# Performance work log

Hardware: AMD Instinct MI355X
Metric: run time of the kernel (lower is better)

Reference implementation:

```python
import jax, jax.numpy as jnp
import numpy as np

N, E, L, H, C, F_IN = 50000, 800000, 3, 8, 16, 128  # nodes, edges, layers, heads, per-head dim, input dim
NEG_SLOPE = 0.2


def setup_inputs() -> dict:
    key = jax.random.key(0)
    k = jax.random.split(key, 8)
    scale = 0.1
    x = jax.random.normal(k[0], (N, F_IN), dtype=jnp.float32)
    Ws = jax.random.normal(k[1], (L, F_IN, H * C), dtype=jnp.float32) * scale
    att_src = jax.random.normal(k[2], (L, H, C), dtype=jnp.float32) * scale
    att_dst = jax.random.normal(k[3], (L, H, C), dtype=jnp.float32) * scale
    biases = jnp.zeros((L, H * C), dtype=jnp.float32)
    fc_w = jax.random.normal(k[4], (H * C, C), dtype=jnp.float32) * scale
    fc_b = jnp.zeros((C,), dtype=jnp.float32)
    edge_index = jax.random.randint(k[5], (2, E), 0, N, dtype=jnp.int64)
    return {"x": x, "Ws": Ws, "att_src": att_src, "att_dst": att_dst,
            "biases": biases, "fc_w": fc_w, "fc_b": fc_b, "edge_index": edge_index}


def _gat_layer(x, W, a_src, a_dst, b, src, dst):
    # x: [N, F]; W: [F, H*C]; a_src/a_dst: [H, C]; src/dst: [E+N] (self-loops included)
    n = x.shape[0]
    h = (x @ W).reshape(n, H, C)                      # [N, H, C]
    e_src = jnp.einsum('nhc,hc->nh', h, a_src)        # [N, H]
    e_dst = jnp.einsum('nhc,hc->nh', h, a_dst)
    e = jax.nn.leaky_relu(e_src[src] + e_dst[dst], NEG_SLOPE)   # [E+N, H]
    # segment softmax over incoming edges of each target node
    emax = jax.ops.segment_max(e, dst, num_segments=n)          # [N, H]
    ex = jnp.exp(e - emax[dst])
    denom = jax.ops.segment_sum(ex, dst, num_segments=n)        # [N, H]
    alpha = ex / (denom[dst] + 1e-16)                            # [E+N, H]
    out = jax.ops.segment_sum(alpha[:, :, None] * h[src], dst, num_segments=n)  # [N, H, C]
    return out.reshape(n, H * C) + b


def reference(x, Ws, att_src, att_dst, biases, fc_w, fc_b, edge_index):
    loop = jnp.arange(N, dtype=edge_index.dtype)
    src = jnp.concatenate([edge_index[0], loop])  # add self-loops (PyG default)
    dst = jnp.concatenate([edge_index[1], loop])
    h = x
    for l in range(L):
        h = _gat_layer(h, Ws[l], att_src[l], att_dst[l], biases[l], src, dst)
        h = jax.nn.elu(h)
    return h @ fc_w + fc_b  # [N, C]
```

## Files before the change

kernel.cpp:

```cpp
#include <hip/hip_runtime.h>
#include <hip/hip_bf16.h>


#define GAT_F 128
#define GAT_H 8
#define GAT_C 16

typedef __attribute__((ext_vector_type(8))) short bf16x8;
typedef __attribute__((ext_vector_type(4))) float f32x4;

__device__ __forceinline__ float bf2f(unsigned short u) {
    union { unsigned int i; float f; } x; x.i = ((unsigned int)u) << 16; return x.f;
}
__device__ __forceinline__ float bfhi2f(unsigned int u) {
    union { unsigned int i; float f; } x; x.i = u & 0xFFFF0000u; return x.f;
}
__device__ __forceinline__ float bflo2f(unsigned int u) {
    union { unsigned int i; float f; } x; x.i = u << 16; return x.f;
}
__device__ __forceinline__ unsigned int pk_bf16(float a, float b) {
    union { float f; unsigned int i; } ua, ub;
    ua.f = a; ub.f = b;
    unsigned int ra = (ua.i + 0x7FFFu + ((ua.i >> 16) & 1u)) >> 16;
    unsigned int rb = (ub.i + 0x7FFFu + ((ub.i >> 16) & 1u)) & 0xFFFF0000u;
    return ra | rb;
}
__device__ __forceinline__ unsigned short f2bf(float a) {
    union { float f; unsigned int i; } ua; ua.f = a;
    return (unsigned short)((ua.i + 0x7FFFu + ((ua.i >> 16) & 1u)) >> 16);
}
__device__ __forceinline__ float ldf(const void* p, size_t i, int isf32) {
    return isf32 ? ((const float*)p)[i] : bf2f(((const unsigned short*)p)[i]);
}
__device__ __forceinline__ int ldei(const int* ei, int i, int is64) {
    return is64 ? ei[2 * (size_t)i] : ei[i];
}

__global__ void k_detect(const unsigned short* __restrict__ xb,
                         const int* __restrict__ ei, int* flags) {
    __shared__ int nan_cnt, zero_cnt;
    if (threadIdx.x == 0) { nan_cnt = 0; zero_cnt = 0; }
    __syncthreads();
    int t = threadIdx.x;
    int ln = 0;
    for (int i = t; i < 8192; i += 256) {
        unsigned short u = xb[i];
        if ((u & 0x7F80) == 0x7F80) ln++;
    }
    int lz = 0;
    for (int i = t; i < 2048; i += 256) {
        if (ei[2 * i + 1] == 0) lz++;
    }
    if (ln) atomicAdd(&nan_cnt, ln);
    if (lz) atomicAdd(&zero_cnt, lz);
    __syncthreads();
    if (t == 0) {
        flags[0] = (nan_cnt > 3) ? 1 : 0;
        flags[1] = (zero_cnt > 1024) ? 1 : 0;
    }
}

__global__ void k_prep(const void* __restrict__ W, const void* __restrict__ asrc,
                       const void* __restrict__ adst,
                       unsigned short* __restrict__ wt, unsigned short* __restrict__ wa,
                       int Lw, const int* __restrict__ flags) {
    int isf32 = flags[0];
    int b = blockIdx.x, t = threadIdx.x;
    if (b < Lw * 64) {
        int gid = b * 256 + t;
        int l = gid >> 14, r = gid & 16383;
        int c = r >> 7, k = r & 127;
        float v = ldf(W, (size_t)l * 16384 + k * 128 + c, isf32);
        wt[gid] = f2bf(v);
    } else {
        int id = (b - Lw * 64) * 256 + t;
        int l = id >> 11, q = id & 2047;
        int j = q >> 7, k = q & 127;
        int head = j & 7;
        const void* av = (j < 8) ? asrc : adst;
        float acc = 0.f;
        #pragma unroll
        for (int cc = 0; cc < 16; cc++) {
            float w = ldf(W, (size_t)l * 16384 + k * 128 + head * 16 + cc, isf32);
            float a = ldf(av, (size_t)l * 128 + head * 16 + cc, isf32);
            acc += w * a;
        }
        wa[id] = f2bf(acc);
    }
}

__global__ void k_init_deg(int* deg, int n) {
    int i = blockIdx.x * 256 + threadIdx.x;
    if (i < n) deg[i] = 1;
}

__global__ void k_count_deg(const int* __restrict__ ei, int* deg, int E,
                            const int* __restrict__ flags) {
    int k = blockIdx.x * 256 + threadIdx.x;
    int is64 = flags[1];
    if (k < E) atomicAdd(&deg[ldei(ei, E + k, is64)], 1);
}

__global__ __launch_bounds__(256) void k_scan_blk(
    const int* __restrict__ deg, int* __restrict__ rp_local,
    int* __restrict__ bsum, int n)
{
    int b = blockIdx.x, t = threadIdx.x;
    int i0 = b * 1024 + t * 4;
    int v0 = 0, v1 = 0, v2 = 0, v3 = 0;
    if (i0 + 3 < n) {
        int4 d = *(const int4*)(deg + i0);
        v0 = d.x; v1 = d.y; v2 = d.z; v3 = d.w;
    } else {
        if (i0     < n) v0 = deg[i0];
        if (i0 + 1 < n) v1 = deg[i0 + 1];
        if (i0 + 2 < n) v2 = deg[i0 + 2];
        if (i0 + 3 < n) v3 = deg[i0 + 3];
    }
    int s = v0 + v1 + v2 + v3;
    int lane = t & 63, wid = t >> 6;
    int sc = s;
    #pragma unroll
    for (int off = 1; off < 64; off <<= 1) {
        int o = __shfl_up(sc, off);
        if (lane >= off) sc += o;
    }
    __shared__ int wsum[4];
    if (lane == 63) wsum[wid] = sc;
    __syncthreads();
    int woff = 0;
    #pragma unroll
    for (int w2 = 0; w2 < 4; w2++) if (w2 < wid) woff += wsum[w2];
    int excl = woff + sc - s;
    if (i0     < n) rp_local[i0]     = excl;
    if (i0 + 1 < n) rp_local[i0 + 1] = excl + v0;
    if (i0 + 2 < n) rp_local[i0 + 2] = excl + v0 + v1;
    if (i0 + 3 < n) rp_local[i0 + 3] = excl + v0 + v1 + v2;
    if (t == 255) bsum[b] = woff + sc;
}

__global__ __launch_bounds__(256) void k_scan_top(
    int* __restrict__ bsum, int* __restrict__ rowptr, int nb, int n)
{
    __shared__ int sh[1024];
    int t = threadIdx.x;
    for (int i = t; i < 1024; i += 256) sh[i] = (i < nb) ? bsum[i] : 0;
    __syncthreads();
    for (int off = 1; off < 1024; off <<= 1) {
        int vals[4];
        #pragma unroll
        for (int k = 0; k < 4; k++) {
            int i = t + 256 * k;
            vals[k] = (i >= off) ? sh[i - off] : 0;
        }
        __syncthreads();
        #pragma unroll
        for (int k = 0; k < 4; k++) sh[t + 256 * k] += vals[k];
        __syncthreads();
    }
    for (int i = t; i < nb; i += 256) bsum[i] = (i == 0) ? 0 : sh[i - 1];
    if (t == 0) rowptr[n] = sh[nb - 1];
}

__global__ void k_place_add(int* __restrict__ rowptr, const int* __restrict__ bsum,
                            int* __restrict__ adj, int* __restrict__ cursor, int n)
{
    int i = blockIdx.x * 256 + threadIdx.x;
    if (i < n) {
        int r = rowptr[i] + bsum[i >> 10];
        rowptr[i] = r;
        adj[r] = i;
        cursor[i] = 1;
    }
    if (blockIdx.x == 0 && threadIdx.x < 8) adj[rowptr[n] + threadIdx.x] = 0;
}

__global__ void k_scatter(const int* __restrict__ ei, const int* __restrict__ rowptr,
                          int* __restrict__ cursor, int* __restrict__ adj, int E,
                          const int* __restrict__ flags) {
    int k = blockIdx.x * 256 + threadIdx.x;
    int is64 = flags[1];
    if (k < E) {
        int s = ldei(ei, k, is64);
        int d = ldei(ei, E + k, is64);
        int p = atomicAdd(&cursor[d], 1);
        adj[rowptr[d] + p] = s;
    }
}

__global__ __launch_bounds__(256) void k_gemm_mfma(
    const void* __restrict__ xin, int x_is_input,
    const unsigned short* __restrict__ wt,
    const unsigned short* __restrict__ wa,
    unsigned int* __restrict__ hb, float* __restrict__ es, float* __restrict__ ed,
    int n, const int* __restrict__ flags)
{
    __shared__ unsigned short xl[64 * 136];
    __shared__ unsigned short wl[144 * 136];
    int isf32 = flags[0];
    int t = threadIdx.x;
    int row0 = blockIdx.x * 64;

    if (isf32 || !x_is_input) {
        const float4* xg = (const float4*)xin;
        for (int i = t; i < 2048; i += 256) {
            int r = i >> 5, c4 = i & 31;
            int gr = row0 + r;
            uint2 u = make_uint2(0u, 0u);
            if (gr < n) {
                float4 v = xg[(size_t)gr * 32 + c4];
                u = make_uint2(pk_bf16(v.x, v.y), pk_bf16(v.z, v.w));
            }
            *(uint2*)&xl[r * 136 + c4 * 4] = u;
        }
    } else {
        const ushort4* xg = (const ushort4*)xin;
        for (int i = t; i < 2048; i += 256) {
            int r = i >> 5, c4 = i & 31;
            int gr = row0 + r;
            ushort4 v = make_ushort4(0, 0, 0, 0);
            if (gr < n) v = xg[(size_t)gr * 32 + c4];
            *(ushort4*)&xl[r * 136 + c4 * 4] = v;
        }
    }
    {
        const ushort4* wg = (const ushort4*)wt;
        for (int i = t; i < 4096; i += 256) {
            int c = i >> 5, k4 = i & 31;
            *(ushort4*)&wl[c * 136 + k4 * 4] = wg[i];
        }
        const ushort4* wag = (const ushort4*)wa;
        for (int i = t; i < 512; i += 256) {
            int j = i >> 5, k4 = i & 31;
            *(ushort4*)&wl[(128 + j) * 136 + k4 * 4] = wag[i];
        }
    }
    __syncthreads();

    int lane = t & 63, wid = t >> 6, quad = lane >> 4, col = lane & 15;
    f32x4 acc[9];
    #pragma unroll
    for (int ct = 0; ct < 9; ct++) acc[ct] = (f32x4){0.f, 0.f, 0.f, 0.f};

    #pragma unroll
    for (int ks = 0; ks < 4; ks++) {
        int k0 = ks * 32;
        bf16x8 af = *(const bf16x8*)&xl[(wid * 16 + col) * 136 + k0 + quad * 8];
        #pragma unroll
        for (int ct = 0; ct < 9; ct++) {
            bf16x8 bf = *(const bf16x8*)&wl[(ct * 16 + col) * 136 + k0 + quad * 8];
            acc[ct] = __builtin_amdgcn_mfma_f32_16x16x32_bf16(af, bf, acc[ct], 0, 0, 0);
        }
    }

    #pragma unroll
    for (int ct = 0; ct < 8; ct++) {
        #pragma unroll
        for (int r = 0; r < 4; r++) {
            int grow = row0 + wid * 16 + quad * 4 + r;
            float v = acc[ct][r];
            float vp = __shfl_xor(v, 1);
            if (!(lane & 1) && grow < n)
                hb[(size_t)grow * 64 + ct * 8 + (col >> 1)] = pk_bf16(v, vp);
        }
    }
    #pragma unroll
    for (int r = 0; r < 4; r++) {
        int grow = row0 + wid * 16 + quad * 4 + r;
        float v = acc[8][r];
        if (grow < n) {
            if (col < 8) es[(size_t)grow * 8 + col] = v;
            else         ed[(size_t)grow * 8 + col - 8] = v;
        }
    }
}

__global__ __launch_bounds__(256) void k_aggregate(
    const unsigned int* __restrict__ hb,
    const float* __restrict__ es, const float* __restrict__ ed,
    const int* __restrict__ rowptr, const int* __restrict__ adj,
    const void* __restrict__ bias, long b_off, float* __restrict__ out, int n,
    const int* __restrict__ flags)
{
    int isf32 = flags[0];
    int lane = threadIdx.x & 63;
    int node = blockIdx.x * 4 + (threadIdx.x >> 6);
    if (node >= n) return;
    int base = rowptr[node];
    int deg = rowptr[node + 1] - base;
    int head = lane >> 3;
    float edv = ed[node * 8 + head];

    float acc0 = 0.f, acc1 = 0.f, lsum = 0.f;
    for (int j0 = 0; j0 < deg; j0 += 4) {
        int sa = adj[base + j0];
        int sb = adj[base + j0 + 1];
        int sc = adj[base + j0 + 2];
        int sd = adj[base + j0 + 3];
        float va = es[sa * 8 + head] + edv;
        float vb = es[sb * 8 + head] + edv;
        float vc = es[sc * 8 + head] + edv;
        float vd = es[sd * 8 + head] + edv;
        unsigned int ha = hb[sa * 64 + lane];
        unsigned int hbv = hb[sb * 64 + lane];
        unsigned int hc = hb[sc * 64 + lane];
        unsigned int hd = hb[sd * 64 + lane];
        va = va > 0.f ? va : 0.2f * va;
        vb = vb > 0.f ? vb : 0.2f * vb;
        vc = vc > 0.f ? vc : 0.2f * vc;
        vd = vd > 0.f ? vd : 0.2f * vd;
        float pa = __expf(va);
        float pb = (j0 + 1 < deg) ? __expf(vb) : 0.f;
        float pc = (j0 + 2 < deg) ? __expf(vc) : 0.f;
        float pd = (j0 + 3 < deg) ? __expf(vd) : 0.f;
        lsum += (pa + pb) + (pc + pd);
        acc0 += pa * bflo2f(ha) + pb * bflo2f(hbv) + pc * bflo2f(hc) + pd * bflo2f(hd);
        acc1 += pa * bfhi2f(ha) + pb * bfhi2f(hbv) + pc * bfhi2f(hc) + pd * bfhi2f(hd);
    }

    float inv = 1.f / (lsum + 1e-16f);
    int ch = lane << 1;
    float o0 = acc0 * inv + ldf(bias, b_off + ch, isf32);
    float o1 = acc1 * inv + ldf(bias, b_off + ch + 1, isf32);
    o0 = o0 > 0.f ? o0 : (__expf(o0) - 1.f);
    o1 = o1 > 0.f ? o1 : (__expf(o1) - 1.f);
    *(float2*)(out + (size_t)node * GAT_F + ch) = make_float2(o0, o1);
}

__global__ __launch_bounds__(256) void k_fc(
    const float* __restrict__ h, const void* __restrict__ fw,
    const void* __restrict__ fb, void* __restrict__ out, int n,
    const int* __restrict__ flags)
{
    __shared__ float fws[GAT_F * GAT_C];
    int isf32 = flags[0];
    int t = threadIdx.x;
    for (int i = t; i < GAT_F * GAT_C; i += 256)
        fws[i] = ldf(fw, i, isf32);
    __syncthreads();
    int row = blockIdx.x * 256 + t;
    if (row >= n) return;
    float acc[16];
    #pragma unroll
    for (int c = 0; c < 16; c++) acc[c] = ldf(fb, c, isf32);
    const float4* hr = (const float4*)(h + (size_t)row * GAT_F);
    for (int k4 = 0; k4 < GAT_F / 4; k4++) {
        float4 xv = hr[k4];
        float xs4[4] = {xv.x, xv.y, xv.z, xv.w};
        #pragma unroll
        for (int kk = 0; kk < 4; kk++) {
            int k = k4 * 4 + kk;
            const float4* wr = (const float4*)(fws + k * GAT_C);
            #pragma unroll
            for (int c4 = 0; c4 < 4; c4++) {
                float4 wv = wr[c4];
                acc[c4 * 4 + 0] += xs4[kk] * wv.x;
                acc[c4 * 4 + 1] += xs4[kk] * wv.y;
                acc[c4 * 4 + 2] += xs4[kk] * wv.z;
                acc[c4 * 4 + 3] += xs4[kk] * wv.w;
            }
        }
    }
    if (isf32) {
        float* o = (float*)out + (size_t)row * GAT_C;
        #pragma unroll
        for (int c = 0; c < 16; c++) o[c] = acc[c];
    } else {
        __hip_bfloat16* o = (__hip_bfloat16*)out + (size_t)row * GAT_C;
        #pragma unroll
        for (int c = 0; c < 16; c++) o[c] = __float2bfloat16(acc[c]);
    }
}

extern "C" void kernel_launch(void* const* d_in, const int* in_sizes, int n_in,
                              void* d_out, int out_size, void* d_ws, size_t ws_size,
                              hipStream_t stream) {
    const void* x      = d_in[0];
    const void* Ws     = d_in[1];
    const void* att_s  = d_in[2];
    const void* att_d  = d_in[3];
    const void* biases = d_in[4];
    const void* fc_w   = d_in[5];
    const void* fc_b   = d_in[6];
    const int*  ei     = (const int*)d_in[7];

    const int N  = in_sizes[0] / GAT_F;
    const int E  = in_sizes[7] / 2;
    const int L  = in_sizes[1] / (GAT_F * GAT_F);
    const int ET = E + N;

    char* w = (char*)d_ws;
    int* flags         = (int*)w;            w += 64;
    float* hA          = (float*)w;          w += (size_t)N * GAT_F * 4;
    unsigned int* hB   = (unsigned int*)w;   w += (size_t)N * 64 * 4;
    float* es          = (float*)w;          w += (size_t)N * GAT_H * 4;
    float* ed          = (float*)w;          w += (size_t)N * GAT_H * 4;
    int* rowptr        = (int*)w;            w += (((size_t)(N + 1) * 4 + 15) & ~15ull);
    int* cursor        = (int*)w;            w += (size_t)N * 4;
    int* bsum          = (int*)w;            w += 1024 * 4;
    int* adj           = (int*)w;            w += (size_t)(ET + 16) * 4;
    unsigned short* wt = (unsigned short*)w; w += (size_t)L * 16384 * 2;
    unsigned short* wa = (unsigned short*)w; w += (size_t)L * 2048 * 2;

    int nb_n = (N + 255) / 256;
    int nb_e = (E + 255) / 256;
    int nb_s = (N + 1023) / 1024;

    k_detect<<<1, 256, 0, stream>>>((const unsigned short*)x, ei, flags);
    k_prep<<<L * 64 + L * 8, 256, 0, stream>>>(Ws, att_s, att_d, wt, wa, L, flags);

    k_init_deg<<<nb_n, 256, 0, stream>>>(cursor, N);
    k_count_deg<<<nb_e, 256, 0, stream>>>(ei, cursor, E, flags);
    k_scan_blk<<<nb_s, 256, 0, stream>>>(cursor, rowptr, bsum, N);
    k_scan_top<<<1, 256, 0, stream>>>(bsum, rowptr, nb_s, N);
    k_place_add<<<nb_n, 256, 0, stream>>>(rowptr, bsum, adj, cursor, N);
    k_scatter<<<nb_e, 256, 0, stream>>>(ei, rowptr, cursor, adj, E, flags);

    int nb_g = (N + 63) / 64;
    int nb_a = (N + 3) / 4;
    for (int l = 0; l < L; l++) {
        k_gemm_mfma<<<nb_g, 256, 0, stream>>>(
            (l == 0) ? x : (const void*)hA, (l == 0) ? 1 : 0,
            wt + (size_t)l * 16384, wa + (size_t)l * 2048,
            hB, es, ed, N, flags);
        k_aggregate<<<nb_a, 256, 0, stream>>>(
            hB, es, ed, rowptr, adj,
            biases, (long)l * GAT_F, hA, N, flags);
    }
    k_fc<<<nb_n, 256, 0, stream>>>(hA, fc_w, fc_b, d_out, N, flags);
}
```

Baseline: 409.0 us.

## Compute per-edge attention weights once per lane and share through LDS

The aggregation kernel now uses one lane per edge to load that edge's source index, gather all 8 head logits with float4 loads, and compute leaky-ReLU and exp for every head. The results go into per-wave LDS buffers. A second inner loop then reads the indices and weights from LDS and gathers the bf16 features as before. This removes the redundant exp and logit gathers that 8 lanes per head used to repeat, and makes the adjacency loads coalesced. The cost is extra LDS traffic, more registers, and a two-phase loop per 64-edge chunk, which relies on intra-wavefront ordering instead of a barrier.

```diff
diff --git a/kernel.cpp b/kernel.cpp
--- a/kernel.cpp
+++ b/kernel.cpp
@@ -282,40 +282,62 @@
     const void* __restrict__ bias, long b_off, float* __restrict__ out, int n,
     const int* __restrict__ flags)
 {
+    __shared__ __align__(16) float alds[4][64 * 12];
+    __shared__ __align__(16) int   slds[4][64];
     int isf32 = flags[0];
     int lane = threadIdx.x & 63;
-    int node = blockIdx.x * 4 + (threadIdx.x >> 6);
+    int wid = threadIdx.x >> 6;
+    int node = blockIdx.x * 4 + wid;
     if (node >= n) return;
     int base = rowptr[node];
     int deg = rowptr[node + 1] - base;
     int head = lane >> 3;
-    float edv = ed[node * 8 + head];
+
+    const float4* es4 = (const float4*)es;
+    const float4* ed4 = (const float4*)ed;
+    float edv[8];
+    {
+        float4 a = ed4[node * 2];
+        float4 b = ed4[node * 2 + 1];
+        edv[0] = a.x; edv[1] = a.y; edv[2] = a.z; edv[3] = a.w;
+        edv[4] = b.x; edv[5] = b.y; edv[6] = b.z; edv[7] = b.w;
+    }
 
     float acc0 = 0.f, acc1 = 0.f, lsum = 0.f;
-    for (int j0 = 0; j0 < deg; j0 += 4) {
-        int sa = adj[base + j0];
-        int sb = adj[base + j0 + 1];
-        int sc = adj[base + j0 + 2];
-        int sd = adj[base + j0 + 3];
-        float va = es[sa * 8 + head] + edv;
-        float vb = es[sb * 8 + head] + edv;
-        float vc = es[sc * 8 + head] + edv;
-        float vd = es[sd * 8 + head] + edv;
-        unsigned int ha = hb[sa * 64 + lane];
-        unsigned int hbv = hb[sb * 64 + lane];
-        unsigned int hc = hb[sc * 64 + lane];
-        unsigned int hd = hb[sd * 64 + lane];
-        va = va > 0.f ? va : 0.2f * va;
-        vb = vb > 0.f ? vb : 0.2f * vb;
-        vc = vc > 0.f ? vc : 0.2f * vc;
-        vd = vd > 0.f ? vd : 0.2f * vd;
-        float pa = __expf(va);
-        float pb = (j0 + 1 < deg) ? __expf(vb) : 0.f;
-        float pc = (j0 + 2 < deg) ? __expf(vc) : 0.f;
-        float pd = (j0 + 3 < deg) ? __expf(vd) : 0.f;
-        lsum += (pa + pb) + (pc + pd);
-        acc0 += pa * bflo2f(ha) + pb * bflo2f(hbv) + pc * bflo2f(hc) + pd * bflo2f(hd);
-        acc1 += pa * bfhi2f(ha) + pb * bfhi2f(hbv) + pc * bfhi2f(hc) + pd * bfhi2f(hd);
+    for (int j0 = 0; j0 < deg; j0 += 64) {
+        int j = j0 + lane;
+        int sp = (j < deg) ? adj[base + j] : 0;
+        float4 ea = es4[sp * 2];
+        float4 eb = es4[sp * 2 + 1];
+        float ev[8] = {ea.x, ea.y, ea.z, ea.w, eb.x, eb.y, eb.z, eb.w};
+        float p[8];
+        #pragma unroll
+        for (int hh = 0; hh < 8; hh++) {
+            float v = ev[hh] + edv[hh];
+            v = fmaxf(v, 0.2f * v);
+            float pe = __expf(v);
+            p[hh] = (j < deg) ? pe : 0.f;
+        }
+        *(float4*)&alds[wid][lane * 12]     = make_float4(p[0], p[1], p[2], p[3]);
+        *(float4*)&alds[wid][lane * 12 + 4] = make_float4(p[4], p[5], p[6], p[7]);
+        slds[wid][lane] = sp;
+        __builtin_amdgcn_s_waitcnt(0);
+
+        int lim = min(64, deg - j0);
+        for (int jj = 0; jj < lim; jj += 4) {
+            int4 sv = *(const int4*)&slds[wid][jj];
+            float a0 = alds[wid][(jj + 0) * 12 + head];
+            float a1 = alds[wid][(jj + 1) * 12 + head];
+            float a2 = alds[wid][(jj + 2) * 12 + head];
+            float a3 = alds[wid][(jj + 3) * 12 + head];
+            unsigned int h0 = hb[sv.x * 64 + lane];
+            unsigned int h1 = hb[sv.y * 64 + lane];
+            unsigned int h2 = hb[sv.z * 64 + lane];
+            unsigned int h3 = hb[sv.w * 64 + lane];
+            lsum += (a0 + a1) + (a2 + a3);
+            acc0 += a0 * bflo2f(h0) + a1 * bflo2f(h1) + a2 * bflo2f(h2) + a3 * bflo2f(h3);
+            acc1 += a0 * bfhi2f(h0) + a1 * bfhi2f(h1) + a2 * bfhi2f(h2) + a3 * bfhi2f(h3);
+        }
     }
 
     float inv = 1.f / (lsum + 1e-16f);
```

Result: faster. 400.6 us (-2.1%).
